# Performance work log

Measured on AMD Instinct MI355X. Metric: run time of the kernel, lower is better.

Reference implementation:

```python
import jax, jax.numpy as jnp
import numpy as np

K = 7
TAU = 0.1
ANCHORS = 512
CANDIDATES = 2048
B, C, H, W = 16, 384, 96, 96
RADIUS = K // 2
K2 = K * K

_dy, _dx = np.meshgrid(np.arange(-RADIUS, RADIUS + 1), np.arange(-RADIUS, RADIUS + 1), indexing='ij')
OFF_Y = jnp.asarray(_dy.reshape(-1).astype(np.int32))  # [K2]
OFF_X = jnp.asarray(_dx.reshape(-1).astype(np.int32))  # [K2]


def _normalize(x):
    # F.normalize(x, dim=1): L2 over channel dim, eps=1e-12
    n = jnp.sqrt(jnp.sum(x * x, axis=1, keepdims=True))
    return x / jnp.maximum(n, 1e-12)


def _local_sims_shared(feat, anchors_yx):
    # feat [B,C,H,W], anchors_yx [M,2] shared across batch -> [B,M,K2]
    ys, xs = anchors_yx[:, 0], anchors_yx[:, 1]          # [M]
    yy = ys[:, None] + OFF_Y[None, :]                    # [M,K2]
    xx = xs[:, None] + OFF_X[None, :]                    # [M,K2]
    center = feat[:, :, ys, xs]                          # [B,C,M]
    neigh = feat[:, :, yy, xx]                           # [B,C,M,K2]
    return jnp.einsum('bcm,bcmk->bmk', center, neigh)


def _local_sims_per_image(feat, anchors_byx):
    # feat [B,C,H,W], anchors_byx [Bm,M,2] per-image anchors -> [B,M,K2]
    b, c, h, w = feat.shape
    flat = feat.reshape(b, c, h * w)
    ys, xs = anchors_byx[..., 0], anchors_byx[..., 1]    # [B,M]
    lin_c = ys * w + xs                                  # [B,M]
    lin_n = (ys[..., None] + OFF_Y) * w + (xs[..., None] + OFF_X)  # [B,M,K2]
    gather = jax.vmap(lambda f, idx: f[:, idx])          # f [C,HW], idx [...]
    center = gather(flat, lin_c)                         # [B,C,M]
    neigh = gather(flat, lin_n)                          # [B,C,M,K2]
    return jnp.einsum('bcm,bcmk->bmk', center, neigh)


def setup_inputs() -> dict:
    key = jax.random.key(0)
    k1, k2, k3, k4 = jax.random.split(key, 4)
    student = jax.random.normal(k1, (B, C, H, W), dtype=jnp.float32)
    teacher = jax.random.normal(k2, (B, C, H, W), dtype=jnp.float32)
    # anchors valid region: [radius, H-radius-1] x [radius, W-radius-1]
    ys = jax.random.randint(k3, (CANDIDATES,), RADIUS, H - RADIUS, dtype=jnp.int32)
    xs = jax.random.randint(k4, (CANDIDATES,), RADIUS, W - RADIUS, dtype=jnp.int32)
    candidate_anchors = jnp.stack([ys, xs], axis=1)      # [Mc,2]
    return {"student": student, "teacher": teacher, "candidate_anchors": candidate_anchors}


def reference(student, teacher, candidate_anchors):
    t_norm = _normalize(teacher)
    # --- teacher-entropy based anchor selection (no_grad in original) ---
    sim_cand = _local_sims_shared(t_norm, candidate_anchors) / TAU   # [B,Mc,K2]
    p = jax.nn.softmax(sim_cand, axis=2)
    ent = -jnp.sum(p * jnp.log(p + 1e-6), axis=2)                    # [B,Mc]
    # per_image=True, kcenter_top_m=0 -> lowest-entropy top-k per image
    _, sel_idx = jax.lax.top_k(-ent, ANCHORS)                        # [B,A]
    anchors = candidate_anchors[sel_idx]                             # [B,A,2]
    # --- local affinity KL ---
    s_norm = _normalize(student)
    sim_s = _local_sims_per_image(s_norm, anchors) / TAU             # [B,A,K2]
    sim_t = _local_sims_per_image(t_norm, anchors) / TAU
    log_ps = jax.nn.log_softmax(sim_s, axis=2)
    log_pt = jax.nn.log_softmax(sim_t, axis=2)
    pt = jnp.exp(log_pt)
    # F.kl_div(log_ps, pt, 'none').sum(2).mean()
    loss = jnp.mean(jnp.sum(pt * (log_pt - log_ps), axis=2))
    return loss
```

## Files before the change

kernel.cpp:

```cpp
#include <hip/hip_runtime.h>
#include <math.h>

#define B 16
#define C 384
#define CPAD 385
#define H 96
#define W 96
#define HW (H*W)
#define M 2048
#define K2 49
#define RAD 3
#define NSEL 512
#define INV_TAU 10.0f
#define TP 32

__device__ inline float wave_max(float v){
  #pragma unroll
  for (int o = 32; o; o >>= 1) v = fmaxf(v, __shfl_xor(v, o));
  return v;
}
__device__ inline float wave_sum(float v){
  #pragma unroll
  for (int o = 32; o; o >>= 1) v += __shfl_xor(v, o);
  return v;
}

__device__ __forceinline__ float patch_sims(const float* __restrict__ img,
                                            int ay, int ax, int lane){
  int g = lane >> 5, t = lane & 31;
  const float4* cp = (const float4*)(img + (size_t)(ay * W + ax) * C) + t;
  float4 c0 = cp[0], c1 = cp[32], c2 = cp[64];
  float mysim = 0.f;
  float4 a0, a1, a2, b0, b1, b2;

#define PLOAD(p0,p1,p2, pp) { \
    int dxl = ((pp) & 3) * 2 + g; if (dxl > 6) dxl = 6; \
    const float4* np = (const float4*)(img + \
        (size_t)((ay + ((pp) >> 2) - RAD) * W + (ax - RAD + dxl)) * C) + t; \
    p0 = np[0]; p1 = np[32]; p2 = np[64]; }

#define PCOMP(p0,p1,p2, pp) { \
    float s0 = c0.x * p0.x; s0 = fmaf(c0.y, p0.y, s0); \
    s0 = fmaf(c0.z, p0.z, s0); s0 = fmaf(c0.w, p0.w, s0); \
    float s1 = c1.x * p1.x; s1 = fmaf(c1.y, p1.y, s1); \
    s1 = fmaf(c1.z, p1.z, s1); s1 = fmaf(c1.w, p1.w, s1); \
    float s2 = c2.x * p2.x; s2 = fmaf(c2.y, p2.y, s2); \
    s2 = fmaf(c2.z, p2.z, s2); s2 = fmaf(c2.w, p2.w, s2); \
    float a = (s0 + s1) + s2; \
    a += __shfl_xor(a, 16); a += __shfl_xor(a, 8); \
    a += __shfl_xor(a, 4);  a += __shfl_xor(a, 2); a += __shfl_xor(a, 1); \
    int kbase = ((pp) >> 2) * 7 + ((pp) & 3) * 2; \
    float v0 = __shfl(a, 0), v1 = __shfl(a, 32); \
    if (lane == kbase) mysim = v0; \
    if (((pp) & 3) < 3 && lane == kbase + 1) mysim = v1; }

  PLOAD(a0,a1,a2, 0);
  #pragma unroll
  for (int pp = 0; pp < 28; pp += 2){
    PLOAD(b0,b1,b2, pp + 1);
    __builtin_amdgcn_sched_barrier(0);
    PCOMP(a0,a1,a2, pp);
    if (pp + 2 < 28) PLOAD(a0,a1,a2, pp + 2);
    __builtin_amdgcn_sched_barrier(0);
    PCOMP(b0,b1,b2, pp + 1);
  }
#undef PLOAD
#undef PCOMP
  return mysim;
}


__global__ void tnorm_kernel(const float* __restrict__ src, float* __restrict__ dst){
  int blk = blockIdx.x;
  int b = blk / (HW / TP);
  int pixbase = (blk % (HW / TP)) * TP;
  __shared__ float tile[TP][CPAD];
  __shared__ float scale[TP];
  const float* sb = src + (size_t)b * C * HW + pixbase;
  int tx = threadIdx.x & 31;
  int ty = threadIdx.x >> 5;
  #pragma unroll 4
  for (int c0 = 0; c0 < C; c0 += 8){
    tile[tx][c0 + ty] = sb[(size_t)(c0 + ty) * HW + tx];
  }
  __syncthreads();
  int pix = threadIdx.x >> 3;
  int j = threadIdx.x & 7;
  float ss = 0.f;
  #pragma unroll 4
  for (int c = j * 48; c < j * 48 + 48; ++c){ float v = tile[pix][c]; ss = fmaf(v, v, ss); }
  ss += __shfl_xor(ss, 1); ss += __shfl_xor(ss, 2); ss += __shfl_xor(ss, 4);
  if (j == 0) scale[pix] = 1.0f / fmaxf(sqrtf(ss), 1e-12f);
  __syncthreads();
  float4* db4 = (float4*)(dst + ((size_t)b * HW + pixbase) * C);
  #pragma unroll 4
  for (int l = threadIdx.x; l < TP * (C / 4); l += 256){
    int p = l / (C / 4), c4 = l - p * (C / 4);
    float s = scale[p];
    float4 v;
    v.x = tile[p][c4 * 4 + 0] * s;
    v.y = tile[p][c4 * 4 + 1] * s;
    v.z = tile[p][c4 * 4 + 2] * s;
    v.w = tile[p][c4 * 4 + 3] * s;
    db4[(size_t)p * (C / 4) + c4] = v;
  }
}

__global__ void sort_kernel(const int* __restrict__ anch, int* __restrict__ order){
  int i = blockIdx.x * 256 + threadIdx.x;
  __shared__ int keys[M];
  for (int j = threadIdx.x; j < M; j += 256){
    int ay = anch[2 * j], ax = anch[2 * j + 1];
    keys[j] = (((ay >> 3) * 12 + (ax >> 3)) << 11) + j;
  }
  __syncthreads();
  int ki = keys[i];
  int r = 0;
  #pragma unroll 4
  for (int j = 0; j < M; ++j) r += (keys[j] < ki) ? 1 : 0;
  order[r] = i;
}

__global__ __launch_bounds__(256, 6) void cand2_kernel(const float* __restrict__ fT,
                             const int* __restrict__ anch, const int* __restrict__ order,
                             float* __restrict__ simc, float* __restrict__ ent){
  int nwg = B * M / 4;
  int bid = blockIdx.x;
  int swz = (bid & 7) * (nwg >> 3) + (bid >> 3);
  int bm = swz * 4 + (threadIdx.x >> 6);
  int b = bm >> 11, mi = bm & (M - 1);
  int lane = threadIdx.x & 63;
  int m = order[mi];
  int ay = anch[2 * m], ax = anch[2 * m + 1];
  const float* img = fT + (size_t)b * HW * C;
  float mysim = patch_sims(img, ay, ax, lane) * INV_TAU;

  float v = (lane < K2) ? mysim : -INFINITY;
  float mx = wave_max(v);
  float e = (lane < K2) ? expf(mysim - mx) : 0.f;
  float se = wave_sum(e);
  float p = e / se;
  float term = (lane < K2) ? (-p * logf(p + 1e-6f)) : 0.f;
  float en = wave_sum(term);
  size_t slot = (size_t)b * M + m;
  if (lane == 0) ent[slot] = en;
  if (lane < K2) simc[slot * K2 + lane] = mysim;
}

__global__ void select_kernel(const float* __restrict__ ent, int* __restrict__ sel){
  int blk = blockIdx.x;
  int b = blk >> 3;
  int i = (blk & 7) * 256 + threadIdx.x;
  __shared__ float se[M];
  for (int j = threadIdx.x; j < M; j += 256) se[j] = ent[b * M + j];
  __syncthreads();
  float ei = se[i];
  int r = 0;
  for (int j = 0; j < M; ++j){
    float ej = se[j];
    r += (ej < ei) || (ej == ei && j < i);
  }
  if (r < NSEL) sel[b * NSEL + r] = i;
}

__global__ void selsort_kernel(const int* __restrict__ anch, const int* __restrict__ sel,
                               int* __restrict__ sel2){
  int b = blockIdx.x;
  __shared__ int keys[NSEL];
  __shared__ int pos[NSEL];
  for (int j = threadIdx.x; j < NSEL; j += 256){
    int m = sel[b * NSEL + j];
    int ay = anch[2 * m], ax = anch[2 * m + 1];
    keys[j] = (((ay >> 3) * 12 + (ax >> 3)) << 11) | m;
    pos[j] = j;
  }
  __syncthreads();
  for (int j = threadIdx.x; j < NSEL; j += 256){
    int kj = keys[j];
    int r = 0;
    #pragma unroll 4
    for (int i = 0; i < NSEL; ++i) r += (keys[i] < kj) ? 1 : 0;
    sel2[b * NSEL + r] = (pos[j] << 11) | (kj & (M - 1));
  }
}

__global__ __launch_bounds__(256, 6) void kl2_kernel(const float* __restrict__ fS,
                           const int* __restrict__ anch,
                           const float* __restrict__ simc, const int* __restrict__ sel2,
                           float* __restrict__ klpart){
  int nwg = B * NSEL / 4;
  int bid = blockIdx.x;
  int swz = (bid & 7) * (nwg >> 3) + (bid >> 3);
  int bj = swz * 4 + (threadIdx.x >> 6);
  int b = bj >> 9, j = bj & (NSEL - 1);
  int lane = threadIdx.x & 63;
  int e2 = sel2[b * NSEL + j];
  int m = e2 & (M - 1), pos = e2 >> 11;
  int ay = anch[2 * m], ax = anch[2 * m + 1];
  const float* img = fS + (size_t)b * HW * C;
  float sim_sv = patch_sims(img, ay, ax, lane) * INV_TAU;
  float sim_tv = (lane < K2) ? simc[((size_t)b * M + m) * K2 + lane] : -INFINITY;

  float vs = (lane < K2) ? sim_sv : -INFINITY;
  float mxs = wave_max(vs);
  float es = (lane < K2) ? expf(sim_sv - mxs) : 0.f;
  float sums = wave_sum(es);
  float ls = sim_sv - mxs - logf(sums);

  float mxt = wave_max(sim_tv);
  float et = (lane < K2) ? expf(sim_tv - mxt) : 0.f;
  float sumt = wave_sum(et);
  float lt = sim_tv - mxt - logf(sumt);

  float pt = et / sumt;
  float term = (lane < K2) ? pt * (lt - ls) : 0.f;
  float kl = wave_sum(term);
  if (lane == 0) klpart[(b << 9) + pos] = kl;
}

__global__ void reduce_kernel(const float* __restrict__ part, float* __restrict__ out){
  float s = 0.f;
  for (int i = threadIdx.x; i < B * NSEL; i += 256) s += part[i];
  s = wave_sum(s);
  __shared__ float wsum[4];
  if ((threadIdx.x & 63) == 0) wsum[threadIdx.x >> 6] = s;
  __syncthreads();
  if (threadIdx.x == 0) out[0] = (wsum[0] + wsum[1] + wsum[2] + wsum[3]) * (1.0f / (B * NSEL));
}


__global__ void norms_kernel(const float* __restrict__ t, const float* __restrict__ s,
                             float* __restrict__ inv_t, float* __restrict__ inv_s){
  int pix = blockIdx.x * blockDim.x + threadIdx.x;
  if (pix >= B * HW) return;
  int b = pix / HW, p = pix - b * HW;
  const float* tb = t + (size_t)b * C * HW + p;
  const float* sb = s + (size_t)b * C * HW + p;
  float at = 0.f, as = 0.f;
  #pragma unroll 4
  for (int c = 0; c < C; ++c){
    float v = tb[(size_t)c * HW]; at = fmaf(v, v, at);
    float u = sb[(size_t)c * HW]; as = fmaf(u, u, as);
  }
  inv_t[pix] = 1.0f / fmaxf(sqrtf(at), 1e-12f);
  inv_s[pix] = 1.0f / fmaxf(sqrtf(as), 1e-12f);
}

__global__ void cand_kernel(const float* __restrict__ t, const int* __restrict__ anch,
                            const float* __restrict__ inv_t,
                            float* __restrict__ simc, float* __restrict__ ent){
  int bm = blockIdx.x;
  int b = bm >> 11, m = bm & (M - 1);
  int lane = threadIdx.x;
  int ay = anch[2 * m], ax = anch[2 * m + 1];
  int k = lane < K2 ? lane : 0;
  int dy = k / 7 - RAD, dx = k - (k / 7) * 7 - RAD;
  int pc = ay * W + ax;
  int pk = (ay + dy) * W + (ax + dx);
  const float* base = t + (size_t)b * C * HW;
  float acc = 0.f;
  #pragma unroll 4
  for (int c = 0; c < C; ++c){
    const float* row = base + (size_t)c * HW;
    acc = fmaf(row[pc], row[pk], acc);
  }
  float sim = acc * inv_t[b * HW + pc] * inv_t[b * HW + pk] * INV_TAU;
  float v = (lane < K2) ? sim : -INFINITY;
  float mx = wave_max(v);
  float e = (lane < K2) ? expf(sim - mx) : 0.f;
  float se = wave_sum(e);
  float p = e / se;
  float term = (lane < K2) ? (-p * logf(p + 1e-6f)) : 0.f;
  float en = wave_sum(term);
  if (lane == 0) ent[bm] = en;
  if (lane < K2) simc[(size_t)bm * K2 + lane] = sim;
}

__global__ void kl_kernel(const float* __restrict__ s, const int* __restrict__ anch,
                          const float* __restrict__ inv_s, const float* __restrict__ simc,
                          const int* __restrict__ sel, float* __restrict__ klpart){
  int bj = blockIdx.x;
  int b = bj >> 9, j = bj & (NSEL - 1);
  int lane = threadIdx.x;
  int m = sel[b * NSEL + j];
  int ay = anch[2 * m], ax = anch[2 * m + 1];
  int k = lane < K2 ? lane : 0;
  int dy = k / 7 - RAD, dx = k - (k / 7) * 7 - RAD;
  int pc = ay * W + ax;
  int pk = (ay + dy) * W + (ax + dx);
  const float* base = s + (size_t)b * C * HW;
  float acc = 0.f;
  #pragma unroll 4
  for (int c = 0; c < C; ++c){
    const float* row = base + (size_t)c * HW;
    acc = fmaf(row[pc], row[pk], acc);
  }
  float sim_sv = acc * inv_s[b * HW + pc] * inv_s[b * HW + pk] * INV_TAU;
  float sim_tv = (lane < K2) ? simc[((size_t)b * M + m) * K2 + lane] : -INFINITY;

  float vs = (lane < K2) ? sim_sv : -INFINITY;
  float mxs = wave_max(vs);
  float es = (lane < K2) ? expf(sim_sv - mxs) : 0.f;
  float sums = wave_sum(es);
  float ls = sim_sv - mxs - logf(sums);

  float mxt = wave_max(sim_tv);
  float et = (lane < K2) ? expf(sim_tv - mxt) : 0.f;
  float sumt = wave_sum(et);
  float lt = sim_tv - mxt - logf(sumt);

  float pt = et / sumt;
  float term = (lane < K2) ? pt * (lt - ls) : 0.f;
  float kl = wave_sum(term);
  if (lane == 0) klpart[bj] = kl;
}

extern "C" void kernel_launch(void* const* d_in, const int* in_sizes, int n_in,
                              void* d_out, int out_size, void* d_ws, size_t ws_size,
                              hipStream_t stream){
  const float* student = (const float*)d_in[0];
  const float* teacher = (const float*)d_in[1];
  const int*   anch    = (const int*)d_in[2];
  float* out = (float*)d_out;

  const size_t fbuf_elems = (size_t)B * HW * C;
  const size_t simc_elems = (size_t)B * M * K2;
  size_t req = (fbuf_elems + simc_elems + (size_t)B * M + (size_t)B * NSEL) * sizeof(float)
             + (2 * (size_t)B * NSEL + (size_t)M) * sizeof(int);

  if (ws_size >= req){
    float* fbuf   = (float*)d_ws;
    float* simc   = fbuf + fbuf_elems;
    float* ent    = simc + simc_elems;
    float* klpart = ent + (size_t)B * M;
    int*   sel    = (int*)(klpart + (size_t)B * NSEL);
    int*   sel2   = sel + (size_t)B * NSEL;
    int*   order  = sel2 + (size_t)B * NSEL;

    hipLaunchKernelGGL(tnorm_kernel, dim3(B * (HW / TP)), dim3(256), 0, stream, teacher, fbuf);
    hipLaunchKernelGGL(sort_kernel, dim3(8), dim3(256), 0, stream, anch, order);
    hipLaunchKernelGGL(cand2_kernel, dim3(B * M / 4), dim3(256), 0, stream,
                       fbuf, anch, order, simc, ent);
    hipLaunchKernelGGL(select_kernel, dim3(B * 8), dim3(256), 0, stream, ent, sel);
    hipLaunchKernelGGL(selsort_kernel, dim3(B), dim3(256), 0, stream, anch, sel, sel2);
    hipLaunchKernelGGL(tnorm_kernel, dim3(B * (HW / TP)), dim3(256), 0, stream, student, fbuf);
    hipLaunchKernelGGL(kl2_kernel, dim3(B * NSEL / 4), dim3(256), 0, stream,
                       fbuf, anch, simc, sel2, klpart);
    hipLaunchKernelGGL(reduce_kernel, dim3(1), dim3(256), 0, stream, klpart, out);
  } else {
    float* ws2    = (float*)d_ws;
    float* inv_t  = ws2;
    float* inv_s  = inv_t + B * HW;
    float* ent    = inv_s + B * HW;
    float* simc   = ent + B * M;
    float* klpart = simc + simc_elems;
    int*   sel    = (int*)(klpart + (size_t)B * NSEL);

    hipLaunchKernelGGL(norms_kernel, dim3((B * HW + 255) / 256), dim3(256), 0, stream,
                       teacher, student, inv_t, inv_s);
    hipLaunchKernelGGL(cand_kernel, dim3(B * M), dim3(64), 0, stream,
                       teacher, anch, inv_t, simc, ent);
    hipLaunchKernelGGL(select_kernel, dim3(B * 8), dim3(256), 0, stream, ent, sel);
    hipLaunchKernelGGL(kl_kernel, dim3(B * NSEL), dim3(64), 0, stream,
                       student, anch, inv_s, simc, sel, klpart);
    hipLaunchKernelGGL(reduce_kernel, dim3(1), dim3(256), 0, stream, klpart, out);
  }
}
```

Baseline: 903.7 us.

## Rewrite normalize-transpose kernel as two-pass chunked scale and raise occupancy bounds

Replaces the transpose-normalize kernel, which staged a whole 32-pixel by 384-channel tile in LDS, with a kernel that first computes per-pixel sums of squares straight from global memory. It then re-reads the input in 96-channel chunks, scales each value and writes it through a smaller padded LDS tile. The smaller LDS footprint over 64-pixel tiles aims to raise occupancy and coalescing, at the cost of reading the input twice. The launch-bounds occupancy hint on the candidate and KL kernels also goes from 6 to 8, which may force register spills.

```diff
diff --git a/kernel.cpp b/kernel.cpp
--- a/kernel.cpp
+++ b/kernel.cpp
@@ -3,7 +3,6 @@
 
 #define B 16
 #define C 384
-#define CPAD 385
 #define H 96
 #define W 96
 #define HW (H*W)
@@ -12,7 +11,8 @@
 #define RAD 3
 #define NSEL 512
 #define INV_TAU 10.0f
-#define TP 32
+#define TSP 64
+#define CCH 96
 
 __device__ inline float wave_max(float v){
   #pragma unroll
@@ -70,39 +70,59 @@
 }
 
 
-__global__ void tnorm_kernel(const float* __restrict__ src, float* __restrict__ dst){
+__global__ __launch_bounds__(256) void tscale2_kernel(const float* __restrict__ src,
+                                                      float* __restrict__ dst){
   int blk = blockIdx.x;
-  int b = blk / (HW / TP);
-  int pixbase = (blk % (HW / TP)) * TP;
-  __shared__ float tile[TP][CPAD];
-  __shared__ float scale[TP];
-  const float* sb = src + (size_t)b * C * HW + pixbase;
-  int tx = threadIdx.x & 31;
-  int ty = threadIdx.x >> 5;
-  #pragma unroll 4
-  for (int c0 = 0; c0 < C; c0 += 8){
-    tile[tx][c0 + ty] = sb[(size_t)(c0 + ty) * HW + tx];
-  }
-  __syncthreads();
-  int pix = threadIdx.x >> 3;
-  int j = threadIdx.x & 7;
-  float ss = 0.f;
-  #pragma unroll 4
-  for (int c = j * 48; c < j * 48 + 48; ++c){ float v = tile[pix][c]; ss = fmaf(v, v, ss); }
-  ss += __shfl_xor(ss, 1); ss += __shfl_xor(ss, 2); ss += __shfl_xor(ss, 4);
-  if (j == 0) scale[pix] = 1.0f / fmaxf(sqrtf(ss), 1e-12f);
-  __syncthreads();
-  float4* db4 = (float4*)(dst + ((size_t)b * HW + pixbase) * C);
-  #pragma unroll 4
-  for (int l = threadIdx.x; l < TP * (C / 4); l += 256){
-    int p = l / (C / 4), c4 = l - p * (C / 4);
-    float s = scale[p];
-    float4 v;
-    v.x = tile[p][c4 * 4 + 0] * s;
-    v.y = tile[p][c4 * 4 + 1] * s;
-    v.z = tile[p][c4 * 4 + 2] * s;
-    v.w = tile[p][c4 * 4 + 3] * s;
-    db4[(size_t)p * (C / 4) + c4] = v;
+  int b = blk / (HW / TSP);
+  int pixbase = (blk % (HW / TSP)) * TSP;
+  __shared__ float tile[TSP][CCH + 1];
+  __shared__ float sspart[4][TSP];
+  __shared__ float scale[TSP];
+  int tx = threadIdx.x & 63;
+  int q  = threadIdx.x >> 6;
+  const float* sb = src + (size_t)b * C * HW + pixbase + tx;
+
+  {
+    float s0 = 0.f, s1 = 0.f;
+    #pragma unroll 8
+    for (int c = 0; c < 48; ++c){
+      float v = sb[(size_t)(q * 96 + c) * HW]; s0 = fmaf(v, v, s0);
+    }
+    #pragma unroll 8
+    for (int c = 48; c < 96; ++c){
+      float v = sb[(size_t)(q * 96 + c) * HW]; s1 = fmaf(v, v, s1);
+    }
+    sspart[q][tx] = s0 + s1;
+  }
+  __syncthreads();
+  if (threadIdx.x < TSP){
+    float ss = (sspart[0][threadIdx.x] + sspart[1][threadIdx.x])
+             + (sspart[2][threadIdx.x] + sspart[3][threadIdx.x]);
+    scale[threadIdx.x] = 1.0f / fmaxf(sqrtf(ss), 1e-12f);
+  }
+  __syncthreads();
+  float sc = scale[tx];
+  float* db = dst + ((size_t)b * HW + pixbase) * C;
+
+  #pragma unroll
+  for (int ch = 0; ch < C / CCH; ++ch){
+    #pragma unroll
+    for (int cc = 0; cc < CCH; cc += 4){
+      tile[tx][cc + q] = sb[(size_t)(ch * CCH + cc + q) * HW] * sc;
+    }
+    __syncthreads();
+    #pragma unroll
+    for (int j = 0; j < 6; ++j){
+      int idx = threadIdx.x + 256 * j;
+      int pix = idx / 24, c4 = idx - pix * 24;
+      float4 v;
+      v.x = tile[pix][c4 * 4 + 0];
+      v.y = tile[pix][c4 * 4 + 1];
+      v.z = tile[pix][c4 * 4 + 2];
+      v.w = tile[pix][c4 * 4 + 3];
+      ((float4*)(db + (size_t)pix * C + ch * CCH))[c4] = v;
+    }
+    __syncthreads();
   }
 }
 
@@ -121,7 +141,7 @@
   order[r] = i;
 }
 
-__global__ __launch_bounds__(256, 6) void cand2_kernel(const float* __restrict__ fT,
+__global__ __launch_bounds__(256, 8) void cand2_kernel(const float* __restrict__ fT,
                              const int* __restrict__ anch, const int* __restrict__ order,
                              float* __restrict__ simc, float* __restrict__ ent){
   int nwg = B * M / 4;
@@ -184,7 +204,7 @@
   }
 }
 
-__global__ __launch_bounds__(256, 6) void kl2_kernel(const float* __restrict__ fS,
+__global__ __launch_bounds__(256, 8) void kl2_kernel(const float* __restrict__ fS,
                            const int* __restrict__ anch,
                            const float* __restrict__ simc, const int* __restrict__ sel2,
                            float* __restrict__ klpart){
@@ -337,13 +357,13 @@
     int*   sel2   = sel + (size_t)B * NSEL;
     int*   order  = sel2 + (size_t)B * NSEL;
 
-    hipLaunchKernelGGL(tnorm_kernel, dim3(B * (HW / TP)), dim3(256), 0, stream, teacher, fbuf);
+    hipLaunchKernelGGL(tscale2_kernel, dim3(B * (HW / TSP)), dim3(256), 0, stream, teacher, fbuf);
     hipLaunchKernelGGL(sort_kernel, dim3(8), dim3(256), 0, stream, anch, order);
     hipLaunchKernelGGL(cand2_kernel, dim3(B * M / 4), dim3(256), 0, stream,
                        fbuf, anch, order, simc, ent);
     hipLaunchKernelGGL(select_kernel, dim3(B * 8), dim3(256), 0, stream, ent, sel);
     hipLaunchKernelGGL(selsort_kernel, dim3(B), dim3(256), 0, stream, anch, sel, sel2);
-    hipLaunchKernelGGL(tnorm_kernel, dim3(B * (HW / TP)), dim3(256), 0, stream, student, fbuf);
+    hipLaunchKernelGGL(tscale2_kernel, dim3(B * (HW / TSP)), dim3(256), 0, stream, student, fbuf);
     hipLaunchKernelGGL(kl2_kernel, dim3(B * NSEL / 4), dim3(256), 0, stream,
                        fbuf, anch, simc, sel2, klpart);
     hipLaunchKernelGGL(reduce_kernel, dim3(1), dim3(256), 0, stream, klpart, out);
```

Result: slower. 1.030 ms (+13.9%).
